# Performance work log

Hardware: AMD Instinct MI355X
Metric: run time of the kernel (lower is better)

Reference implementation:

```python
import jax, jax.numpy as jnp
import numpy as np

N = 50000      # nodes
F_IN = 500     # in_channels
MID = 64       # mid_layer_channel
H = 2          # heads
OUT = 40       # out_channels
E = 800000     # edges per order
ORDER = 3
NEG_SLOPE = 0.2


def _gat(x, edge_index, W, a_src, a_dst, b, concat):
    # PyG-style GATConv (eval mode, dropout off), with self loops.
    n = x.shape[0]
    heads, ch = a_src.shape
    h = (x @ W).reshape(n, heads, ch)                    # [N,H,C]
    loop = jnp.arange(n)
    src = jnp.concatenate([edge_index[0], loop])
    dst = jnp.concatenate([edge_index[1], loop])
    al_s = jnp.sum(h * a_src, axis=-1)                   # [N,H]
    al_d = jnp.sum(h * a_dst, axis=-1)                   # [N,H]
    e = jax.nn.leaky_relu(al_s[src] + al_d[dst], NEG_SLOPE)   # [Etot,H]
    m = jax.ops.segment_max(e, dst, num_segments=n)      # softmax over incoming edges per dst
    ex = jnp.exp(e - m[dst])
    den = jax.ops.segment_sum(ex, dst, num_segments=n)
    alpha = ex / (den[dst] + 1e-16)
    out = jax.ops.segment_sum(alpha[:, :, None] * h[src], dst, num_segments=n)  # [N,H,C]
    if concat:
        return out.reshape(n, heads * ch) + b
    return out.mean(axis=1) + b


def _aggr(states, Wmix, wfin):
    # NOrderAggrConv (depth=2): mix order states with [order,order] weights + ELU,
    # then reduce to a single state with a learned [order] combination.
    h = jnp.stack(states, axis=1)                        # [N,order,C]
    h = jax.nn.elu(jnp.einsum('nkc,kj->njc', h, Wmix))
    return jnp.einsum('nkc,k->nc', h, wfin)


def setup_inputs():
    key = jax.random.key(0)
    ks = jax.random.split(key, 40)
    d = {}
    d['node_feature'] = jax.random.normal(ks[0], (N, F_IN), jnp.float32)
    for o in range(ORDER):
        d[f'adj{o}'] = jax.random.randint(ks[1 + o], (2, E), 0, N)
    i = 4
    s = 0.05
    layer_dims = [(F_IN, MID, H * MID), (MID * H, OUT, OUT)]
    for l, (fin, c, bdim) in enumerate(layer_dims):
        for o in range(ORDER):
            d[f'W_{l}_{o}'] = jax.random.normal(ks[i], (fin, H * c), jnp.float32) * s; i += 1
            d[f'as_{l}_{o}'] = jax.random.normal(ks[i], (H, c), jnp.float32) * s; i += 1
            d[f'ad_{l}_{o}'] = jax.random.normal(ks[i], (H, c), jnp.float32) * s; i += 1
            d[f'b_{l}_{o}'] = jnp.zeros((bdim,), jnp.float32)
    for l in range(2):
        d[f'agg{l}_W'] = jax.random.normal(ks[i], (ORDER, ORDER), jnp.float32) * 0.5; i += 1
        d[f'agg{l}_w'] = jnp.full((ORDER,), 1.0 / ORDER, jnp.float32)
    return d


def reference(node_feature, adj0, adj1, adj2,
              W_0_0, as_0_0, ad_0_0, b_0_0,
              W_0_1, as_0_1, ad_0_1, b_0_1,
              W_0_2, as_0_2, ad_0_2, b_0_2,
              W_1_0, as_1_0, ad_1_0, b_1_0,
              W_1_1, as_1_1, ad_1_1, b_1_1,
              W_1_2, as_1_2, ad_1_2, b_1_2,
              agg0_W, agg0_w, agg1_W, agg1_w):
    adjs = (adj0, adj1, adj2)
    p0 = ((W_0_0, as_0_0, ad_0_0, b_0_0),
          (W_0_1, as_0_1, ad_0_1, b_0_1),
          (W_0_2, as_0_2, ad_0_2, b_0_2))
    p1 = ((W_1_0, as_1_0, ad_1_0, b_1_0),
          (W_1_1, as_1_1, ad_1_1, b_1_1),
          (W_1_2, as_1_2, ad_1_2, b_1_2))
    aggs = ((agg0_W, agg0_w), (agg1_W, agg1_w))
    x = node_feature  # eval mode: dropout is identity
    for l, params in enumerate((p0, p1)):
        concat = (l == 0)
        states = [jax.nn.elu(_gat(x, adjs[o], *params[o], concat)) for o in range(ORDER)]
        x = _aggr(states, *aggs[l])
    return jax.nn.log_softmax(x, axis=1)
```

## Files before the change

kernel.cpp:

```cpp
#include <hip/hip_runtime.h>
#include <cstdint>
#include <cstddef>
#include <math.h>


typedef __attribute__((ext_vector_type(8))) short short8;
typedef __attribute__((ext_vector_type(4))) float f32x4;
typedef __attribute__((ext_vector_type(2))) float f32x2;
typedef unsigned int u32x2 __attribute__((ext_vector_type(2)));

struct P3f { const float* p[3]; };
struct P3c { const int* p[3]; };

__device__ __forceinline__ float leakyf(float x) { return x > 0.f ? x : 0.2f * x; }
__device__ __forceinline__ float eluf(float x)   { return x > 0.f ? x : expm1f(x); }

__device__ __forceinline__ unsigned short bf16r(float x) {
  unsigned int u = __float_as_uint(x);
  u += 0x7fffu + ((u >> 16) & 1u);
  return (unsigned short)(u >> 16);
}
__device__ __forceinline__ float bflo(unsigned int u) { return __uint_as_float(u << 16); }
__device__ __forceinline__ float bfhi(unsigned int u) { return __uint_as_float(u & 0xffff0000u); }

__device__ __forceinline__ float fold32v(float v) {
#if __has_builtin(__builtin_amdgcn_permlane32_swap)
  u32x2 r = __builtin_amdgcn_permlane32_swap(__float_as_uint(v), __float_as_uint(v), false, false);
  return __uint_as_float(r[1]);
#else
  return __shfl_xor(v, 32, 64);
#endif
}
__device__ __forceinline__ float fold16v(float v) {
#if __has_builtin(__builtin_amdgcn_permlane16_swap)
  u32x2 r = __builtin_amdgcn_permlane16_swap(__float_as_uint(v), __float_as_uint(v), false, false);
  return __uint_as_float(r[1]);
#else
  return __uint_as_float((unsigned int)__builtin_amdgcn_ds_swizzle(
      (int)__float_as_uint(v), 0x401F));
#endif
}

__device__ __forceinline__ void bf8_fma2(uint4 q, float xx, f32x2* a) {
  f32x2 v0 = {bflo(q.x), bfhi(q.x)};
  f32x2 v1 = {bflo(q.y), bfhi(q.y)};
  f32x2 v2 = {bflo(q.z), bfhi(q.z)};
  f32x2 v3 = {bflo(q.w), bfhi(q.w)};
  a[0] += xx * v0;
  a[1] += xx * v1;
  a[2] += xx * v2;
  a[3] += xx * v3;
}

__global__ __launch_bounds__(256) void zero_int_kernel(int* p, int n) {
  int i = blockIdx.x * blockDim.x + threadIdx.x;
  if (i < n) p[i] = 0;
}

__global__ __launch_bounds__(256) void convA_kernel(const float* __restrict__ A,
    unsigned short* __restrict__ Ab, int M, int K, int Kpad) {
  int i = blockIdx.x * blockDim.x + threadIdx.x;
  int row = i >> 6;
  int koff = (i & 63) * 8;
  if (row >= M) return;
  const float* ap = A + (size_t)row * K;
  unsigned short v[8];
  if (koff + 8 <= K) {
    float4 q0 = ((const float4*)(ap + koff))[0];
    float4 q1 = ((const float4*)(ap + koff))[1];
    v[0] = bf16r(q0.x); v[1] = bf16r(q0.y); v[2] = bf16r(q0.z); v[3] = bf16r(q0.w);
    v[4] = bf16r(q1.x); v[5] = bf16r(q1.y); v[6] = bf16r(q1.z); v[7] = bf16r(q1.w);
  } else {
#pragma unroll
    for (int k = 0; k < 8; ++k)
      v[k] = (koff + k < K) ? bf16r(ap[koff + k]) : (unsigned short)0;
  }
  *(uint4*)(Ab + (size_t)row * Kpad + koff) = *(const uint4*)v;
}

__global__ __launch_bounds__(256) void count3_kernel(P3c adj, int* __restrict__ cntb,
                                                     int E, int N) {
  int i = blockIdx.x * blockDim.x + threadIdx.x;
  int o = blockIdx.y;
  if (i < E) atomicAdd(&cntb[o * N + adj.p[o][E + i]], 1);
}

#define SCAN_T 256
#define SCAN_VPT 8
#define SCAN_TILE 2048

__global__ __launch_bounds__(SCAN_T) void scan1_kernel(const int* __restrict__ cntb,
    int* __restrict__ rowptrb, int* __restrict__ bsums, int N) {
  __shared__ int lds[SCAN_T];
  const int o = blockIdx.y;
  const int* cnt = cntb + o * N;
  int* rowptr = rowptrb + o * (N + 1);
  int t = threadIdx.x;
  int base = blockIdx.x * SCAN_TILE + t * SCAN_VPT;
  int v[SCAN_VPT];
  int s = 0;
#pragma unroll
  for (int i = 0; i < SCAN_VPT; ++i) {
    int idx = base + i;
    int x = (idx < N) ? cnt[idx] : 0;
    s += x;
    v[i] = s;
  }
  lds[t] = s;
  __syncthreads();
  for (int off = 1; off < SCAN_T; off <<= 1) {
    int add = (t >= off) ? lds[t - off] : 0;
    __syncthreads();
    lds[t] += add;
    __syncthreads();
  }
  int excl = (t > 0) ? lds[t - 1] : 0;
#pragma unroll
  for (int i = 0; i < SCAN_VPT; ++i) {
    int idx = base + i;
    if (idx < N) rowptr[idx + 1] = excl + v[i];
  }
  if (t == SCAN_T - 1) bsums[o * 64 + blockIdx.x] = lds[t];
}

__global__ void scan2_kernel(int* bsums, int nb, int* rowptrb, int N) {
  if (threadIdx.x == 0 && blockIdx.x == 0) {
    for (int o = 0; o < 3; ++o) {
      int run = 0;
      for (int i = 0; i < nb; ++i) {
        int x = bsums[o * 64 + i];
        bsums[o * 64 + i] = run;
        run += x;
      }
      rowptrb[o * (N + 1)] = 0;
    }
  }
}

__global__ __launch_bounds__(256) void scan3_kernel(int* __restrict__ rowptrb,
    const int* __restrict__ bsums, int N) {
  int idx = blockIdx.x * blockDim.x + threadIdx.x;
  int o = blockIdx.y;
  if (idx < N) rowptrb[o * (N + 1) + idx + 1] += bsums[o * 64 + idx / SCAN_TILE];
}

__global__ __launch_bounds__(256) void fill3_kernel(P3c adj,
    const int* __restrict__ rowptrb, int* __restrict__ curb,
    int* __restrict__ colvb, int E, int N) {
  int i = blockIdx.x * blockDim.x + threadIdx.x;
  int o = blockIdx.y;
  if (i < E) {
    const int* a = adj.p[o];
    int d = a[E + i];
    int pos = atomicAdd(&curb[o * N + d], 1);
    colvb[(size_t)o * E + rowptrb[o * (N + 1) + d] + pos] = a[i];
  }
}

__global__ __launch_bounds__(256) void conv_bt3_kernel(P3f W,
    unsigned short* __restrict__ BtB, int K, int NC, int Kpad) {
  int n = blockIdx.y;
  int o = blockIdx.z;
  int k = blockIdx.x * 256 + threadIdx.x;
  if (k >= Kpad) return;
  float v = (k < K) ? W.p[o][(size_t)k * NC + n] : 0.f;
  BtB[(size_t)o * NC * Kpad + (size_t)n * Kpad + k] = bf16r(v);
}

#define GBM 128
#define LDSTRIDE 40

template<int NT>
__global__ __launch_bounds__(256) void mfma_gemm_kernel(
    const unsigned short* __restrict__ Ab, const unsigned short* __restrict__ BtB,
    P3f asp, P3f adp, unsigned short* __restrict__ CbB,
    float2* __restrict__ alsB, float2* __restrict__ aldB, int M, int Kpad) {
  constexpr int NC = NT * 16;
  constexpr int CH = NT * 8;
  __shared__ unsigned short As[GBM * LDSTRIDE];
  __shared__ unsigned short Bs[NC * LDSTRIDE];
  const int t = threadIdx.x;
  const int o = blockIdx.y;
  const int wave = t >> 6, lane = t & 63;
  const int quad = lane >> 4, l16 = lane & 15;
  const int m0 = blockIdx.x * GBM;
  const unsigned short* Bt = BtB + (size_t)o * NC * Kpad;
  unsigned short* Cb = CbB + (size_t)o * M * NC;
  float2* al_s = alsB + (size_t)o * M;
  float2* al_d = aldB + (size_t)o * M;
  const float* a_src = asp.p[o];
  const float* a_dst = adp.p[o];

  f32x4 acc[2][NT];
#pragma unroll
  for (int i = 0; i < 2; ++i)
#pragma unroll
    for (int j = 0; j < NT; ++j) acc[i][j] = (f32x4){0.f, 0.f, 0.f, 0.f};

  const int arow = t >> 1;
  const int akoff = (t & 1) * 16;
  const int gm = m0 + arow;
  const unsigned short* arowp = Ab + (size_t)gm * Kpad;
  const unsigned short* browp = Bt + (size_t)arow * Kpad;

  for (int k0 = 0; k0 < Kpad; k0 += 32) {
    if (k0) __syncthreads();
    const int kb = k0 + akoff;
    {
      uint4 q0 = {0, 0, 0, 0}, q1 = {0, 0, 0, 0};
      if (gm < M) {
        const uint4* p = (const uint4*)(arowp + kb);
        q0 = p[0]; q1 = p[1];
      }
      short8* dst = (short8*)&As[arow * LDSTRIDE + akoff];
      union { uint4 q; short8 s; } c0, c1;
      c0.q = q0; c1.q = q1;
      dst[0] = c0.s;
      dst[1] = c1.s;
    }
    if (arow < NC) {
      const uint4* p = (const uint4*)(browp + kb);
      uint4 q0 = p[0], q1 = p[1];
      short8* dst = (short8*)&Bs[arow * LDSTRIDE + akoff];
      union { uint4 q; short8 s; } c0, c1;
      c0.q = q0; c1.q = q1;
      dst[0] = c0.s;
      dst[1] = c1.s;
    }
    __syncthreads();
    short8 af[2];
#pragma unroll
    for (int rt = 0; rt < 2; ++rt)
      af[rt] = *(const short8*)&As[(wave * 32 + rt * 16 + l16) * LDSTRIDE + quad * 8];
    short8 bfv[NT];
#pragma unroll
    for (int ct = 0; ct < NT; ++ct)
      bfv[ct] = *(const short8*)&Bs[(ct * 16 + l16) * LDSTRIDE + quad * 8];
#pragma unroll
    for (int rt = 0; rt < 2; ++rt)
#pragma unroll
      for (int ct = 0; ct < NT; ++ct)
        acc[rt][ct] = __builtin_amdgcn_mfma_f32_16x16x32_bf16(af[rt], bfv[ct],
                                                              acc[rt][ct], 0, 0, 0);
  }
  float asv[NT], adv[NT];
#pragma unroll
  for (int ct = 0; ct < NT; ++ct) {
    int col = ct * 16 + l16;
    asv[ct] = a_src[col];
    adv[ct] = a_dst[col];
  }
#pragma unroll
  for (int rt = 0; rt < 2; ++rt) {
    int gr0 = m0 + wave * 32 + rt * 16 + quad * 4;
#pragma unroll
    for (int r = 0; r < 4; ++r) {
      int gr = gr0 + r;
      float ps0 = 0.f, ps1 = 0.f, pd0 = 0.f, pd1 = 0.f;
#pragma unroll
      for (int ct = 0; ct < NT; ++ct) {
        int col = ct * 16 + l16;
        float v = acc[rt][ct][r];
        if (gr < M) Cb[(size_t)gr * NC + col] = bf16r(v);
        if (col < CH) { ps0 += v * asv[ct]; pd0 += v * adv[ct]; }
        else          { ps1 += v * asv[ct]; pd1 += v * adv[ct]; }
      }
#pragma unroll
      for (int off = 1; off < 16; off <<= 1) {
        ps0 += __shfl_xor(ps0, off, 64);
        ps1 += __shfl_xor(ps1, off, 64);
        pd0 += __shfl_xor(pd0, off, 64);
        pd1 += __shfl_xor(pd1, off, 64);
      }
      if (l16 == 0 && gr < M) {
        al_s[gr] = make_float2(ps0, ps1);
        al_d[gr] = make_float2(pd0, pd1);
      }
    }
  }
}

template<int C, int CONCAT>
__global__ __launch_bounds__(256) void gat_direct_kernel(
    const unsigned short* __restrict__ hB, const float2* __restrict__ alsB,
    const float2* __restrict__ aldB, const int* __restrict__ rowptrB,
    const int* __restrict__ colvB, P3f biasp, unsigned short* __restrict__ outB,
    int N, int E) {
  constexpr int HC = 2 * C;
  constexpr int FLd = HC / 8;
  constexpr int HB = C / 8;
  constexpr int OW = CONCAT ? HC : C;
  const int o = blockIdx.y;
  const unsigned short* h = hB + (size_t)o * N * HC;
  const float2* al_s = alsB + (size_t)o * N;
  const float2* al_d = aldB + (size_t)o * N;
  const int* rowptr = rowptrB + o * (N + 1);
  const float* bias = biasp.p[o];
  unsigned short* out = outB + (size_t)o * N * OW;

  const int w = (blockIdx.x * blockDim.x + threadIdx.x) >> 6;
  const int lane = threadIdx.x & 63;
  if (w >= N) return;
  const int eslot = lane >> 4;
  const int f4 = lane & 15;
  const bool hl = f4 < FLd;

  const float2 ad = al_d[w];
  const float2 asf = al_s[w];
  const int beg = rowptr[w], end = rowptr[w + 1];
  const int* colv = colvB + (size_t)o * E;

  const float xs0 = __expf(leakyf(asf.x + ad.x));
  const float xs1 = __expf(leakyf(asf.y + ad.y));

  uint4 qself = make_uint4(0, 0, 0, 0);
  if (lane < FLd) qself = ((const uint4*)(h + (size_t)w * HC))[f4];

  f32x2 acc[4] = {}, acc2[4] = {};
  float dp0 = 0.f, dp1 = 0.f;

  for (int e0 = beg; e0 < end; e0 += 16) {
    const int ea = e0 + eslot;
    const int eb = ea + 4;
    const int ec = ea + 8;
    const int ed = ea + 12;
    const bool va = ea < end, vb = eb < end, vc = ec < end, vd = ed < end;
    const int sa = va ? colv[ea] : 0;
    const int sb = vb ? colv[eb] : 0;
    const int sc = vc ? colv[ec] : 0;
    const int sd = vd ? colv[ed] : 0;
    uint4 qa = make_uint4(0, 0, 0, 0), qb = qa, qc = qa, qd = qa;
    if (hl) {
      qa = ((const uint4*)(h + (size_t)sa * HC))[f4];
      qb = ((const uint4*)(h + (size_t)sb * HC))[f4];
      qc = ((const uint4*)(h + (size_t)sc * HC))[f4];
      qd = ((const uint4*)(h + (size_t)sd * HC))[f4];
    }
    const float2 aa = al_s[sa];
    const float2 ab = al_s[sb];
    const float2 ac = al_s[sc];
    const float2 adx = al_s[sd];
    const float xa0 = va ? __expf(leakyf(aa.x + ad.x)) : 0.f;
    const float xa1 = va ? __expf(leakyf(aa.y + ad.y)) : 0.f;
    const float xb0 = vb ? __expf(leakyf(ab.x + ad.x)) : 0.f;
    const float xb1 = vb ? __expf(leakyf(ab.y + ad.y)) : 0.f;
    const float xc0 = vc ? __expf(leakyf(ac.x + ad.x)) : 0.f;
    const float xc1 = vc ? __expf(leakyf(ac.y + ad.y)) : 0.f;
    const float xd0 = vd ? __expf(leakyf(adx.x + ad.x)) : 0.f;
    const float xd1 = vd ? __expf(leakyf(adx.y + ad.y)) : 0.f;
    dp0 += (xa0 + xb0) + (xc0 + xd0);
    dp1 += (xa1 + xb1) + (xc1 + xd1);
    if (hl) {
      bf8_fma2(qa, (f4 < HB) ? xa0 : xa1, acc);
      bf8_fma2(qb, (f4 < HB) ? xb0 : xb1, acc2);
      bf8_fma2(qc, (f4 < HB) ? xc0 : xc1, acc);
      bf8_fma2(qd, (f4 < HB) ? xd0 : xd1, acc2);
    }
  }

#pragma unroll
  for (int i = 0; i < 4; ++i) acc[i] += acc2[i];

#pragma unroll
  for (int i = 0; i < 4; ++i) {
    acc[i][0] += fold32v(acc[i][0]);
    acc[i][1] += fold32v(acc[i][1]);
  }
  dp0 += fold32v(dp0);
  dp1 += fold32v(dp1);
#pragma unroll
  for (int i = 0; i < 4; ++i) {
    acc[i][0] += fold16v(acc[i][0]);
    acc[i][1] += fold16v(acc[i][1]);
  }
  dp0 += fold16v(dp0);
  dp1 += fold16v(dp1);

  const float den0 = dp0 + xs0, den1 = dp1 + xs1;

  if (lane < FLd) bf8_fma2(qself, (f4 < HB) ? xs0 : xs1, acc);

  const float inv0 = 1.f / (den0 + 1e-16f), inv1 = 1.f / (den1 + 1e-16f);
  if (CONCAT) {
    if (lane < FLd) {
      const float xx = (f4 < HB) ? inv0 : inv1;
      const float* bp = bias + f4 * 8;
      unsigned int pk[4];
#pragma unroll
      for (int i = 0; i < 4; ++i) {
        unsigned short lo = bf16r(eluf(acc[i][0] * xx + bp[2 * i]));
        unsigned short hi = bf16r(eluf(acc[i][1] * xx + bp[2 * i + 1]));
        pk[i] = (unsigned int)lo | ((unsigned int)hi << 16);
      }
      ((uint4*)(out + (size_t)w * OW + f4 * 8))[0] = make_uint4(pk[0], pk[1], pk[2], pk[3]);
    }
  } else {
    float p[8];
#pragma unroll
    for (int i = 0; i < 4; ++i) {
      p[2 * i]     = __shfl(acc[i][0], lane + HB, 64);
      p[2 * i + 1] = __shfl(acc[i][1], lane + HB, 64);
    }
    if (lane < HB) {
      const float* bp = bias + f4 * 8;
      unsigned int pk[4];
#pragma unroll
      for (int i = 0; i < 4; ++i) {
        float v0 = 0.5f * (acc[i][0] * inv0 + p[2 * i] * inv1) + bp[2 * i];
        float v1 = 0.5f * (acc[i][1] * inv0 + p[2 * i + 1] * inv1) + bp[2 * i + 1];
        pk[i] = (unsigned int)bf16r(eluf(v0)) | ((unsigned int)bf16r(eluf(v1)) << 16);
      }
      ((uint4*)(out + (size_t)w * OW + f4 * 8))[0] = make_uint4(pk[0], pk[1], pk[2], pk[3]);
    }
  }
}

template<int BF16OUT>
__global__ __launch_bounds__(256) void mixb_kernel(const unsigned short* __restrict__ sb,
    const float* __restrict__ Wm, const float* __restrict__ wf,
    void* __restrict__ out, int perU) {
  int i = blockIdx.x * blockDim.x + threadIdx.x;
  if (i >= perU) return;
  const unsigned int* sp = (const unsigned int*)sb;
  unsigned int u0 = sp[i];
  unsigned int u1 = sp[perU + i];
  unsigned int u2 = sp[2 * perU + i];
  float a0 = bflo(u0), a1 = bfhi(u0);
  float b0 = bflo(u1), b1 = bfhi(u1);
  float c0 = bflo(u2), c1 = bfhi(u2);
  float r0 = 0.f, r1 = 0.f;
#pragma unroll
  for (int j = 0; j < 3; ++j) {
    float w0 = Wm[j], w1 = Wm[3 + j], w2 = Wm[6 + j], wj = wf[j];
    r0 += wj * eluf(a0 * w0 + b0 * w1 + c0 * w2);
    r1 += wj * eluf(a1 * w0 + b1 * w1 + c1 * w2);
  }
  if (BF16OUT) {
    ((unsigned int*)out)[i] = (unsigned int)bf16r(r0) | ((unsigned int)bf16r(r1) << 16);
  } else {
    ((float2*)out)[i] = make_float2(r0, r1);
  }
}

__global__ __launch_bounds__(256) void log_softmax_kernel(const float* __restrict__ x,
    float* __restrict__ out, int N, int C) {
  int w = (blockIdx.x * blockDim.x + threadIdx.x) >> 6;
  int lane = threadIdx.x & 63;
  if (w >= N) return;
  float v = (lane < C) ? x[(size_t)w * C + lane] : -INFINITY;
  float mx = v;
#pragma unroll
  for (int off = 1; off < 64; off <<= 1) mx = fmaxf(mx, __shfl_xor(mx, off, 64));
  float ex = (lane < C) ? expf(v - mx) : 0.f;
  float s = ex;
#pragma unroll
  for (int off = 1; off < 64; off <<= 1) s += __shfl_xor(s, off, 64);
  if (lane < C) out[(size_t)w * C + lane] = v - mx - logf(s);
}

extern "C" void kernel_launch(void* const* d_in, const int* in_sizes, int n_in,
                              void* d_out, int out_size, void* d_ws, size_t ws_size,
                              hipStream_t stream) {
  const int F_IN = 500;
  const int N = in_sizes[0] / F_IN;
  const int E = in_sizes[1] / 2;
  const int HC0 = 128;
  const int HC1 = 80;
  const int C1 = 40;
  const int K0pad = 512, K1pad = 128;

  const float* x0 = (const float*)d_in[0];
  P3c adj;
  adj.p[0] = (const int*)d_in[1];
  adj.p[1] = (const int*)d_in[2];
  adj.p[2] = (const int*)d_in[3];
  P3f W0p, as0p, ad0p, b0p, W1p, as1p, ad1p, b1p;
  for (int o = 0; o < 3; ++o) {
    W0p.p[o]  = (const float*)d_in[4 + 4 * o + 0];
    as0p.p[o] = (const float*)d_in[4 + 4 * o + 1];
    ad0p.p[o] = (const float*)d_in[4 + 4 * o + 2];
    b0p.p[o]  = (const float*)d_in[4 + 4 * o + 3];
    W1p.p[o]  = (const float*)d_in[16 + 4 * o + 0];
    as1p.p[o] = (const float*)d_in[16 + 4 * o + 1];
    ad1p.p[o] = (const float*)d_in[16 + 4 * o + 2];
    b1p.p[o]  = (const float*)d_in[16 + 4 * o + 3];
  }
  const float* agg0W = (const float*)d_in[28];
  const float* agg0w = (const float*)d_in[29];
  const float* agg1W = (const float*)d_in[30];
  const float* agg1w = (const float*)d_in[31];

  char* ws = (char*)d_ws;
  size_t off = 0;
  auto alloc = [&](size_t bytes) -> void* {
    off = (off + 255) & ~(size_t)255;
    void* p = ws + off;
    off += bytes;
    return p;
  };
  int* rowptrb = (int*)alloc((size_t)3 * (N + 1) * 4);
  int* colvb   = (int*)alloc((size_t)3 * E * 4);
  int* cntcur  = (int*)alloc((size_t)6 * N * 4);
  int* bsums   = (int*)alloc(3 * 64 * 4);
  unsigned short* x0b = (unsigned short*)alloc((size_t)N * K0pad * 2);
  unsigned short* hB  = (unsigned short*)alloc((size_t)3 * N * HC0 * 2);
  unsigned short* stB = (unsigned short*)alloc((size_t)3 * N * HC0 * 2);
  float* x2 = (float*)alloc((size_t)N * C1 * 4);
  float2* alsB = (float2*)alloc((size_t)3 * N * 8);
  float2* aldB = (float2*)alloc((size_t)3 * N * 8);
  unsigned short* Bt0B = (unsigned short*)alloc((size_t)3 * HC0 * K0pad * 2);
  unsigned short* Bt1B = (unsigned short*)alloc((size_t)3 * HC1 * K1pad * 2);
  (void)ws_size;

  const int TB = 256;
  const int nbE = (E + TB - 1) / TB;
  const int nbN = (N + TB - 1) / TB;
  const int scanBlocks = (N + SCAN_TILE - 1) / SCAN_TILE;
  const int waveBlocks = (int)(((size_t)N * 64 + TB - 1) / TB);
  const int gemmBlocks = (N + GBM - 1) / GBM;

  convA_kernel<<<(int)(((size_t)N * 64 + TB - 1) / TB), TB, 0, stream>>>(
      x0, x0b, N, F_IN, K0pad);
  conv_bt3_kernel<<<dim3((K0pad + 255) / 256, HC0, 3), TB, 0, stream>>>(W0p, Bt0B, F_IN, HC0, K0pad);
  conv_bt3_kernel<<<dim3((K1pad + 255) / 256, HC1, 3), TB, 0, stream>>>(W1p, Bt1B, HC0, HC1, K1pad);

  zero_int_kernel<<<(6 * N + TB - 1) / TB, TB, 0, stream>>>(cntcur, 6 * N);
  count3_kernel<<<dim3(nbE, 3), TB, 0, stream>>>(adj, cntcur, E, N);
  scan1_kernel<<<dim3(scanBlocks, 3), SCAN_T, 0, stream>>>(cntcur, rowptrb, bsums, N);
  scan2_kernel<<<1, 64, 0, stream>>>(bsums, scanBlocks, rowptrb, N);
  scan3_kernel<<<dim3(nbN, 3), TB, 0, stream>>>(rowptrb, bsums, N);
  fill3_kernel<<<dim3(nbE, 3), TB, 0, stream>>>(adj, rowptrb, cntcur + 3 * N, colvb, E, N);

  mfma_gemm_kernel<8><<<dim3(gemmBlocks, 3), TB, 0, stream>>>(
      x0b, Bt0B, as0p, ad0p, hB, alsB, aldB, N, K0pad);
  gat_direct_kernel<64, 1><<<dim3(waveBlocks, 3), TB, 0, stream>>>(
      hB, alsB, aldB, rowptrb, colvb, b0p, stB, N, E);
  mixb_kernel<1><<<((N * HC0 / 2) + TB - 1) / TB, TB, 0, stream>>>(
      stB, agg0W, agg0w, stB, N * HC0 / 2);

  mfma_gemm_kernel<5><<<dim3(gemmBlocks, 3), TB, 0, stream>>>(
      stB, Bt1B, as1p, ad1p, hB, alsB, aldB, N, K1pad);
  gat_direct_kernel<40, 0><<<dim3(waveBlocks, 3), TB, 0, stream>>>(
      hB, alsB, aldB, rowptrb, colvb, b1p, stB, N, E);
  mixb_kernel<0><<<((N * C1 / 2) + TB - 1) / TB, TB, 0, stream>>>(
      stB, agg1W, agg1w, x2, N * C1 / 2);

  log_softmax_kernel<<<waveBlocks, TB, 0, stream>>>(x2, (float*)d_out, N, C1);
}
```

Baseline: 903.1 us.

## Precompute per-edge attention weights and pack four destination nodes per wave

Adds an edge-parallel kernel that computes exp(leaky(als[src]+ald[dst])) per CSR edge, using a new dst array written by fill, and stores the result in the reused x0b buffer. The aggregation kernel now gives each 16-lane quarter-wave its own destination node instead of spreading one node's edges across the full wave, which removes the cross-lane fold reductions. The aim is to cut the exp and al_s gather work from the inner loop and to make better use of lanes when the degree is around 16. The trade-offs are extra global traffic for dst and alpha, and load imbalance because each wave loops up to the largest degree among its four nodes.

After: 847.3 us. -6.2%, faster.

```diff
diff --git a/kernel.cpp b/kernel.cpp
--- a/kernel.cpp
+++ b/kernel.cpp
@@ -7,7 +7,6 @@
 typedef __attribute__((ext_vector_type(8))) short short8;
 typedef __attribute__((ext_vector_type(4))) float f32x4;
 typedef __attribute__((ext_vector_type(2))) float f32x2;
-typedef unsigned int u32x2 __attribute__((ext_vector_type(2)));
 
 struct P3f { const float* p[3]; };
 struct P3c { const int* p[3]; };
@@ -22,24 +21,6 @@
 }
 __device__ __forceinline__ float bflo(unsigned int u) { return __uint_as_float(u << 16); }
 __device__ __forceinline__ float bfhi(unsigned int u) { return __uint_as_float(u & 0xffff0000u); }
-
-__device__ __forceinline__ float fold32v(float v) {
-#if __has_builtin(__builtin_amdgcn_permlane32_swap)
-  u32x2 r = __builtin_amdgcn_permlane32_swap(__float_as_uint(v), __float_as_uint(v), false, false);
-  return __uint_as_float(r[1]);
-#else
-  return __shfl_xor(v, 32, 64);
-#endif
-}
-__device__ __forceinline__ float fold16v(float v) {
-#if __has_builtin(__builtin_amdgcn_permlane16_swap)
-  u32x2 r = __builtin_amdgcn_permlane16_swap(__float_as_uint(v), __float_as_uint(v), false, false);
-  return __uint_as_float(r[1]);
-#else
-  return __uint_as_float((unsigned int)__builtin_amdgcn_ds_swizzle(
-      (int)__float_as_uint(v), 0x401F));
-#endif
-}
 
 __device__ __forceinline__ void bf8_fma2(uint4 q, float xx, f32x2* a) {
   f32x2 v0 = {bflo(q.x), bfhi(q.x)};
@@ -146,15 +127,33 @@
 
 __global__ __launch_bounds__(256) void fill3_kernel(P3c adj,
     const int* __restrict__ rowptrb, int* __restrict__ curb,
-    int* __restrict__ colvb, int E, int N) {
+    int* __restrict__ colvb, int* __restrict__ dstvb, int E, int N) {
   int i = blockIdx.x * blockDim.x + threadIdx.x;
   int o = blockIdx.y;
   if (i < E) {
     const int* a = adj.p[o];
     int d = a[E + i];
     int pos = atomicAdd(&curb[o * N + d], 1);
-    colvb[(size_t)o * E + rowptrb[o * (N + 1) + d] + pos] = a[i];
-  }
+    size_t idx = (size_t)o * E + rowptrb[o * (N + 1) + d] + pos;
+    colvb[idx] = a[i];
+    dstvb[idx] = d;
+  }
+}
+
+__global__ __launch_bounds__(256) void alpha3_kernel(const int* __restrict__ colvb,
+    const int* __restrict__ dstvb, const float2* __restrict__ alsB,
+    const float2* __restrict__ aldB, float2* __restrict__ alphB, int E, int N) {
+  int i = blockIdx.x * blockDim.x + threadIdx.x;
+  int o = blockIdx.y;
+  if (i >= E) return;
+  size_t base = (size_t)o * E + i;
+  int s = colvb[base];
+  int d = dstvb[base];
+  const float2* als = alsB + (size_t)o * N;
+  const float2* ald = aldB + (size_t)o * N;
+  float2 a = als[s];
+  float2 b = ald[d];
+  alphB[base] = make_float2(__expf(leakyf(a.x + b.x)), __expf(leakyf(a.y + b.y)));
 }
 
 __global__ __launch_bounds__(256) void conv_bt3_kernel(P3f W,
@@ -281,11 +280,11 @@
 }
 
 template<int C, int CONCAT>
-__global__ __launch_bounds__(256) void gat_direct_kernel(
+__global__ __launch_bounds__(256) void gat_slot4_kernel(
     const unsigned short* __restrict__ hB, const float2* __restrict__ alsB,
     const float2* __restrict__ aldB, const int* __restrict__ rowptrB,
-    const int* __restrict__ colvB, P3f biasp, unsigned short* __restrict__ outB,
-    int N, int E) {
+    const int* __restrict__ colvB, const float2* __restrict__ alphB,
+    P3f biasp, unsigned short* __restrict__ outB, int N, int E) {
   constexpr int HC = 2 * C;
   constexpr int FLd = HC / 8;
   constexpr int HB = C / 8;
@@ -295,94 +294,76 @@
   const float2* al_s = alsB + (size_t)o * N;
   const float2* al_d = aldB + (size_t)o * N;
   const int* rowptr = rowptrB + o * (N + 1);
+  const int* colv = colvB + (size_t)o * E;
+  const float2* alph = alphB + (size_t)o * E;
   const float* bias = biasp.p[o];
   unsigned short* out = outB + (size_t)o * N * OW;
 
-  const int w = (blockIdx.x * blockDim.x + threadIdx.x) >> 6;
+  const int gw = (blockIdx.x * blockDim.x + threadIdx.x) >> 6;
   const int lane = threadIdx.x & 63;
-  if (w >= N) return;
-  const int eslot = lane >> 4;
+  const int slot = lane >> 4;
   const int f4 = lane & 15;
+  const int w = gw * 4 + slot;
+  if (gw * 4 >= N) return;
+  const bool vn = w < N;
+  const int wc = vn ? w : N - 1;
   const bool hl = f4 < FLd;
 
-  const float2 ad = al_d[w];
-  const float2 asf = al_s[w];
-  const int beg = rowptr[w], end = rowptr[w + 1];
-  const int* colv = colvB + (size_t)o * E;
-
+  const int beg = rowptr[wc];
+  const int deg = vn ? (rowptr[wc + 1] - beg) : 0;
+  int md = deg;
+  md = max(md, __shfl_xor(md, 32, 64));
+  md = max(md, __shfl_xor(md, 16, 64));
+
+  const float2 ad = al_d[wc];
+  const float2 asf = al_s[wc];
   const float xs0 = __expf(leakyf(asf.x + ad.x));
   const float xs1 = __expf(leakyf(asf.y + ad.y));
-
-  uint4 qself = make_uint4(0, 0, 0, 0);
-  if (lane < FLd) qself = ((const uint4*)(h + (size_t)w * HC))[f4];
+  float dp0 = xs0, dp1 = xs1;
 
   f32x2 acc[4] = {}, acc2[4] = {};
-  float dp0 = 0.f, dp1 = 0.f;
-
-  for (int e0 = beg; e0 < end; e0 += 16) {
-    const int ea = e0 + eslot;
-    const int eb = ea + 4;
-    const int ec = ea + 8;
-    const int ed = ea + 12;
-    const bool va = ea < end, vb = eb < end, vc = ec < end, vd = ed < end;
-    const int sa = va ? colv[ea] : 0;
-    const int sb = vb ? colv[eb] : 0;
-    const int sc = vc ? colv[ec] : 0;
-    const int sd = vd ? colv[ed] : 0;
-    uint4 qa = make_uint4(0, 0, 0, 0), qb = qa, qc = qa, qd = qa;
+  if (hl) {
+    uint4 q = ((const uint4*)(h + (size_t)wc * HC))[f4];
+    bf8_fma2(q, (f4 < HB) ? xs0 : xs1, acc);
+  }
+
+  const float2 z2 = make_float2(0.f, 0.f);
+  for (int t = 0; t < md; t += 4) {
+    const int j0 = beg + t;
+    const bool v0 = t < deg;
+    const bool v1 = t + 1 < deg;
+    const bool v2 = t + 2 < deg;
+    const bool v3 = t + 3 < deg;
+    const int s0 = v0 ? colv[j0] : 0;
+    const int s1 = v1 ? colv[j0 + 1] : 0;
+    const int s2 = v2 ? colv[j0 + 2] : 0;
+    const int s3 = v3 ? colv[j0 + 3] : 0;
+    const float2 a0 = v0 ? alph[j0] : z2;
+    const float2 a1 = v1 ? alph[j0 + 1] : z2;
+    const float2 a2 = v2 ? alph[j0 + 2] : z2;
+    const float2 a3 = v3 ? alph[j0 + 3] : z2;
+    uint4 q0 = make_uint4(0, 0, 0, 0), q1 = q0, q2 = q0, q3 = q0;
     if (hl) {
-      qa = ((const uint4*)(h + (size_t)sa * HC))[f4];
-      qb = ((const uint4*)(h + (size_t)sb * HC))[f4];
-      qc = ((const uint4*)(h + (size_t)sc * HC))[f4];
-      qd = ((const uint4*)(h + (size_t)sd * HC))[f4];
-    }
-    const float2 aa = al_s[sa];
-    const float2 ab = al_s[sb];
-    const float2 ac = al_s[sc];
-    const float2 adx = al_s[sd];
-    const float xa0 = va ? __expf(leakyf(aa.x + ad.x)) : 0.f;
-    const float xa1 = va ? __expf(leakyf(aa.y + ad.y)) : 0.f;
-    const float xb0 = vb ? __expf(leakyf(ab.x + ad.x)) : 0.f;
-    const float xb1 = vb ? __expf(leakyf(ab.y + ad.y)) : 0.f;
-    const float xc0 = vc ? __expf(leakyf(ac.x + ad.x)) : 0.f;
-    const float xc1 = vc ? __expf(leakyf(ac.y + ad.y)) : 0.f;
-    const float xd0 = vd ? __expf(leakyf(adx.x + ad.x)) : 0.f;
-    const float xd1 = vd ? __expf(leakyf(adx.y + ad.y)) : 0.f;
-    dp0 += (xa0 + xb0) + (xc0 + xd0);
-    dp1 += (xa1 + xb1) + (xc1 + xd1);
+      q0 = ((const uint4*)(h + (size_t)s0 * HC))[f4];
+      q1 = ((const uint4*)(h + (size_t)s1 * HC))[f4];
+      q2 = ((const uint4*)(h + (size_t)s2 * HC))[f4];
+      q3 = ((const uint4*)(h + (size_t)s3 * HC))[f4];
+    }
+    dp0 += (a0.x + a1.x) + (a2.x + a3.x);
+    dp1 += (a0.y + a1.y) + (a2.y + a3.y);
     if (hl) {
-      bf8_fma2(qa, (f4 < HB) ? xa0 : xa1, acc);
-      bf8_fma2(qb, (f4 < HB) ? xb0 : xb1, acc2);
-      bf8_fma2(qc, (f4 < HB) ? xc0 : xc1, acc);
-      bf8_fma2(qd, (f4 < HB) ? xd0 : xd1, acc2);
-    }
-  }
-
+      bf8_fma2(q0, (f4 < HB) ? a0.x : a0.y, acc);
+      bf8_fma2(q1, (f4 < HB) ? a1.x : a1.y, acc2);
+      bf8_fma2(q2, (f4 < HB) ? a2.x : a2.y, acc);
+      bf8_fma2(q3, (f4 < HB) ? a3.x : a3.y, acc2);
+    }
+  }
 #pragma unroll
   for (int i = 0; i < 4; ++i) acc[i] += acc2[i];
 
-#pragma unroll
-  for (int i = 0; i < 4; ++i) {
-    acc[i][0] += fold32v(acc[i][0]);
-    acc[i][1] += fold32v(acc[i][1]);
-  }
-  dp0 += fold32v(dp0);
-  dp1 += fold32v(dp1);
-#pragma unroll
-  for (int i = 0; i < 4; ++i) {
-    acc[i][0] += fold16v(acc[i][0]);
-    acc[i][1] += fold16v(acc[i][1]);
-  }
-  dp0 += fold16v(dp0);
-  dp1 += fold16v(dp1);
-
-  const float den0 = dp0 + xs0, den1 = dp1 + xs1;
-
-  if (lane < FLd) bf8_fma2(qself, (f4 < HB) ? xs0 : xs1, acc);
-
-  const float inv0 = 1.f / (den0 + 1e-16f), inv1 = 1.f / (den1 + 1e-16f);
+  const float inv0 = 1.f / (dp0 + 1e-16f), inv1 = 1.f / (dp1 + 1e-16f);
   if (CONCAT) {
-    if (lane < FLd) {
+    if (vn && hl) {
       const float xx = (f4 < HB) ? inv0 : inv1;
       const float* bp = bias + f4 * 8;
       unsigned int pk[4];
@@ -401,7 +382,7 @@
       p[2 * i]     = __shfl(acc[i][0], lane + HB, 64);
       p[2 * i + 1] = __shfl(acc[i][1], lane + HB, 64);
     }
-    if (lane < HB) {
+    if (vn && f4 < HB) {
       const float* bp = bias + f4 * 8;
       unsigned int pk[4];
 #pragma unroll
@@ -500,6 +481,7 @@
   };
   int* rowptrb = (int*)alloc((size_t)3 * (N + 1) * 4);
   int* colvb   = (int*)alloc((size_t)3 * E * 4);
+  int* dstvb   = (int*)alloc((size_t)3 * E * 4);
   int* cntcur  = (int*)alloc((size_t)6 * N * 4);
   int* bsums   = (int*)alloc(3 * 64 * 4);
   unsigned short* x0b = (unsigned short*)alloc((size_t)N * K0pad * 2);
@@ -510,14 +492,16 @@
   float2* aldB = (float2*)alloc((size_t)3 * N * 8);
   unsigned short* Bt0B = (unsigned short*)alloc((size_t)3 * HC0 * K0pad * 2);
   unsigned short* Bt1B = (unsigned short*)alloc((size_t)3 * HC1 * K1pad * 2);
+  float2* alphb = (float2*)x0b;
   (void)ws_size;
 
   const int TB = 256;
   const int nbE = (E + TB - 1) / TB;
   const int nbN = (N + TB - 1) / TB;
   const int scanBlocks = (N + SCAN_TILE - 1) / SCAN_TILE;
-  const int waveBlocks = (int)(((size_t)N * 64 + TB - 1) / TB);
   const int gemmBlocks = (N + GBM - 1) / GBM;
+  const int slot4Blocks = (int)(((size_t)((N + 3) / 4) * 64 + TB - 1) / TB);
+  const int lsBlocks = (int)(((size_t)N * 64 + TB - 1) / TB);
 
   convA_kernel<<<(int)(((size_t)N * 64 + TB - 1) / TB), TB, 0, stream>>>(
       x0, x0b, N, F_IN, K0pad);
@@ -529,21 +513,23 @@
   scan1_kernel<<<dim3(scanBlocks, 3), SCAN_T, 0, stream>>>(cntcur, rowptrb, bsums, N);
   scan2_kernel<<<1, 64, 0, stream>>>(bsums, scanBlocks, rowptrb, N);
   scan3_kernel<<<dim3(nbN, 3), TB, 0, stream>>>(rowptrb, bsums, N);
-  fill3_kernel<<<dim3(nbE, 3), TB, 0, stream>>>(adj, rowptrb, cntcur + 3 * N, colvb, E, N);
+  fill3_kernel<<<dim3(nbE, 3), TB, 0, stream>>>(adj, rowptrb, cntcur + 3 * N, colvb, dstvb, E, N);
 
   mfma_gemm_kernel<8><<<dim3(gemmBlocks, 3), TB, 0, stream>>>(
       x0b, Bt0B, as0p, ad0p, hB, alsB, aldB, N, K0pad);
-  gat_direct_kernel<64, 1><<<dim3(waveBlocks, 3), TB, 0, stream>>>(
-      hB, alsB, aldB, rowptrb, colvb, b0p, stB, N, E);
+  alpha3_kernel<<<dim3(nbE, 3), TB, 0, stream>>>(colvb, dstvb, alsB, aldB, alphb, E, N);
+  gat_slot4_kernel<64, 1><<<dim3(slot4Blocks, 3), TB, 0, stream>>>(
+      hB, alsB, aldB, rowptrb, colvb, alphb, b0p, stB, N, E);
   mixb_kernel<1><<<((N * HC0 / 2) + TB - 1) / TB, TB, 0, stream>>>(
       stB, agg0W, agg0w, stB, N * HC0 / 2);
 
   mfma_gemm_kernel<5><<<dim3(gemmBlocks, 3), TB, 0, stream>>>(
       stB, Bt1B, as1p, ad1p, hB, alsB, aldB, N, K1pad);
-  gat_direct_kernel<40, 0><<<dim3(waveBlocks, 3), TB, 0, stream>>>(
-      hB, alsB, aldB, rowptrb, colvb, b1p, stB, N, E);
+  alpha3_kernel<<<dim3(nbE, 3), TB, 0, stream>>>(colvb, dstvb, alsB, aldB, alphb, E, N);
+  gat_slot4_kernel<40, 0><<<dim3(slot4Blocks, 3), TB, 0, stream>>>(
+      hB, alsB, aldB, rowptrb, colvb, alphb, b1p, stB, N, E);
   mixb_kernel<0><<<((N * C1 / 2) + TB - 1) / TB, TB, 0, stream>>>(
       stB, agg1W, agg1w, x2, N * C1 / 2);
 
-  log_softmax_kernel<<<waveBlocks, TB, 0, stream>>>(x2, (float*)d_out, N, C1);
-}
+  log_softmax_kernel<<<lsBlocks, TB, 0, stream>>>(x2, (float*)d_out, N, C1);
+}
```
